# Performance work log

Hardware: AMD Instinct MI355X
Metric: run time of the kernel (lower is better)

## Reference

```python
import jax, jax.numpy as jnp
import numpy as np
from jax import lax

NEG = -1e9
B, H, C, TX, TY = 4, 256, 80, 256, 1024  # batch, hidden, mel bins, text len, mel len


def setup_inputs() -> dict:
    key = jax.random.key(0)
    k = jax.random.split(key, 6)
    en = jax.random.normal(k[0], (B, H, TX), jnp.float32)
    mu = jax.random.normal(k[1], (B, C, TX), jnp.float32)
    log_sigma = 0.1 * jax.random.normal(k[2], (B, C, TX), jnp.float32)
    y = jax.random.normal(k[3], (B, C, TY), jnp.float32)
    x_lengths = jax.random.randint(k[4], (B,), TX // 2, TX + 1, jnp.int32)
    y_lengths = jax.random.randint(k[5], (B,), TY // 2, TY + 1, jnp.int32)
    return {"en": en, "mu": mu, "log_sigma": log_sigma, "y": y,
            "x_lengths": x_lengths, "y_lengths": y_lengths}


def sequence_mask(lengths, max_len):
    return jnp.arange(max_len)[None, :] < lengths[:, None]


def compute_log_probs(mu, log_sigma, y):
    # y: [B,C,Ty] -> [B,1,Ty,C]; mu/log_sigma: [B,C,Tx] -> [B,Tx,1,C]
    yb = jnp.transpose(y, (0, 2, 1))[:, None]
    mub = jnp.transpose(mu, (0, 2, 1))[:, :, None]
    lsb = jnp.transpose(log_sigma, (0, 2, 1))[:, :, None]
    # mse / sigma^2 = (y-mu)^2 * exp(-2*log_sigma); mean over channel dim
    expo = -0.5 * jnp.mean((yb - mub) ** 2 * jnp.exp(-2.0 * lsb), axis=-1)  # [B,Tx,Ty]
    return expo - 0.5 * jnp.mean(lsb, axis=-1)  # broadcast [B,Tx,1] -> [B,Tx,Ty]


def maximum_path(logp, mask, x_lengths, y_lengths):
    """Monotonic alignment search (Glow-TTS Viterbi DP), vectorized over batch."""
    b, tx, ty = logp.shape
    lp = jnp.where(mask > 0, logp, NEG)
    cols = jnp.moveaxis(lp, 2, 0)  # [Ty, B, Tx]
    v0 = jnp.broadcast_to(jnp.where(jnp.arange(tx) == 0, 0.0, NEG), (b, tx)).astype(logp.dtype)

    def fwd(v, col):
        v_shift = jnp.concatenate([jnp.full((b, 1), NEG, v.dtype), v[:, :-1]], axis=1)
        diag = v_shift > v  # come from (x-1, y-1) rather than (x, y-1)
        return col + jnp.maximum(v, v_shift), diag

    _, diags = lax.scan(fwd, v0, cols)  # diags: [Ty, B, Tx] bool

    xs_idx = jnp.arange(tx)

    def bwd(idx, inp):
        yv, dcol = inp
        active = yv < y_lengths  # [B]
        row = (xs_idx[None, :] == idx[:, None]) & active[:, None]
        d = jnp.take_along_axis(dcol, idx[:, None], axis=1)[:, 0]
        idx = jnp.where(active & (idx > 0) & d, idx - 1, idx)
        return idx, row

    _, rows = lax.scan(bwd, x_lengths - 1, (jnp.arange(ty), diags), reverse=True)
    return lax.stop_gradient(jnp.moveaxis(rows, 0, 2).astype(logp.dtype))  # [B,Tx,Ty]


def generate_path(dr, mask):
    # dr: [B,Tx] durations; mask: [B,Tx,Ty]
    ty = mask.shape[-1]
    cum = jnp.cumsum(dr, axis=1)
    pm = (jnp.arange(ty)[None, None, :] < cum[:, :, None]).astype(dr.dtype)
    path = pm - jnp.pad(pm, ((0, 0), (1, 0), (0, 0)))[:, :-1]
    return path * mask


def reference(en, mu, log_sigma, y, x_lengths, y_lengths):
    tx, ty = mu.shape[-1], y.shape[-1]
    x_mask = sequence_mask(x_lengths, tx).astype(jnp.float32)  # [B,Tx]
    y_mask = sequence_mask(y_lengths, ty).astype(jnp.float32)  # [B,Ty]
    attn_mask = x_mask[:, :, None] * y_mask[:, None, :]        # [B,Tx,Ty]
    logp = compute_log_probs(mu, log_sigma, y)
    attn = maximum_path(logp, attn_mask, x_lengths, y_lengths)
    dr_mas = jnp.sum(attn, axis=-1)                            # durations [B,Tx]
    path = generate_path(dr_mas, attn_mask)                    # convert_dr_to_align
    # expand_encoder_outputs: attn^T @ en^T -> [B,H,Ty]
    o_en_ex = jnp.einsum('bxy,bhx->bhy', path, en)
    return o_en_ex, logp, attn, dr_mas
```

## Files before the change

### kernel.cpp

```cpp
#include <hip/hip_runtime.h>
#include <cstdint>
#include <cmath>

#define B_ 4
#define H_ 256
#define C_ 80
#define TX_ 256
#define TY_ 1024
#define NEGF (-1e9f)

#define OFF_LOGP (B_*H_*TY_)
#define OFF_ATTN (OFF_LOGP + B_*TX_*TY_)
#define OFF_DR   (OFF_ATTN + B_*TX_*TY_)

__device__ __forceinline__ float dpp_shr1_negfill_f32(float x) {
  union { float f; int i; } u, o, r;
  u.f = x; o.f = NEGF;
  r.i = __builtin_amdgcn_update_dpp(o.i, u.i, 0x138, 0xf, 0xf, false);
  return r.f;
}

__global__ __launch_bounds__(256) void k_logp(
    const float* __restrict__ mu, const float* __restrict__ ls,
    const float* __restrict__ y, const int* __restrict__ xlp,
    const int* __restrict__ ylp, float* __restrict__ logp_out,
    float* __restrict__ lpT)
{
  const int b  = blockIdx.y;
  const int x0 = blockIdx.x * 4;
  const int tid = threadIdx.x;
  __shared__ double s_w[4][C_];
  __shared__ double s_m1[4][C_];
  __shared__ double s_wm2[4][C_];
  __shared__ double s_lsv[4][C_];
  __shared__ double s_K[4];
  __shared__ double s_t0[4];
  __shared__ float tile[TY_][4];
  for (int i = tid; i < 4 * C_; i += 256) {
    int xi = i / C_, c = i - xi * C_;
    double m = (double)mu[(b * C_ + c) * TX_ + x0 + xi];
    double l = (double)ls[(b * C_ + c) * TX_ + x0 + xi];
    double w = exp(-2.0 * l);
    s_w[xi][c]   = w;
    s_m1[xi][c]  = -2.0 * w * m;
    s_wm2[xi][c] = w * m * m;
    s_lsv[xi][c] = l;
  }
  __syncthreads();
  {
    int xi = tid >> 6, cc = tid & 63;
    double kp = (cc < C_) ? s_wm2[xi][cc] : 0.0;
    double tp = (cc < C_) ? s_lsv[xi][cc] : 0.0;
    if (cc + 64 < C_) { kp += s_wm2[xi][cc + 64]; tp += s_lsv[xi][cc + 64]; }
#pragma unroll
    for (int off = 32; off; off >>= 1) {
      kp += __shfl_down(kp, off);
      tp += __shfl_down(tp, off);
    }
    if (cc == 0) { s_K[xi] = kp; s_t0[xi] = -0.5 * (tp * (1.0 / C_)); }
  }
  __syncthreads();

  const int t0 = tid * 4;
  double acc[4][4];
#pragma unroll
  for (int xi = 0; xi < 4; ++xi)
#pragma unroll
    for (int k = 0; k < 4; ++k) acc[xi][k] = 0.0;

  const float4* yp = (const float4*)(y + (size_t)b * C_ * TY_) + tid;
#pragma unroll 4
  for (int c = 0; c < C_; ++c) {
    float4 yv = yp[c * (TY_ / 4)];
    double y0 = yv.x, y1 = yv.y, y2 = yv.z, y3 = yv.w;
#pragma unroll
    for (int xi = 0; xi < 4; ++xi) {
      double w = s_w[xi][c], m1 = s_m1[xi][c];
      double u0 = fma(w, y0, m1), u1 = fma(w, y1, m1);
      double u2 = fma(w, y2, m1), u3 = fma(w, y3, m1);
      acc[xi][0] = fma(u0, y0, acc[xi][0]);
      acc[xi][1] = fma(u1, y1, acc[xi][1]);
      acc[xi][2] = fma(u2, y2, acc[xi][2]);
      acc[xi][3] = fma(u3, y3, acc[xi][3]);
    }
  }

  const int xlen = xlp[b], ylen = ylp[b];
#pragma unroll
  for (int xi = 0; xi < 4; ++xi) {
    int x = x0 + xi;
    double c0 = s_t0[xi], K = s_K[xi];
    float r[4];
#pragma unroll
    for (int k = 0; k < 4; ++k)
      r[k] = (float)((acc[xi][k] + K) * (-0.5 / C_) + c0);
    *(float4*)&logp_out[((size_t)(b * TX_ + x)) * TY_ + t0] =
        make_float4(r[0], r[1], r[2], r[3]);
    bool xm = x < xlen;
#pragma unroll
    for (int k = 0; k < 4; ++k)
      tile[t0 + k][xi] = (xm && (t0 + k) < ylen) ? r[k] : NEGF;
  }
  __syncthreads();

  float* dst = lpT + (size_t)b * TY_ * TX_ + x0;
  const float4* tp = (const float4*)tile;
#pragma unroll
  for (int k = 0; k < 4; ++k) {
    int t = tid + 256 * k;
    *(float4*)&dst[(size_t)t * TX_] = tp[t];
  }
}

__global__ __launch_bounds__(64, 1) void k_dp(
    const float* __restrict__ lpT, const int* __restrict__ xlp,
    const int* __restrict__ ylp, float* __restrict__ dr_out,
    int* __restrict__ cum_ws, int* __restrict__ xt_ws)
{
  const int b = blockIdx.x;
  const int tid = threadIdx.x;
  const int lane = tid;
  __shared__ __align__(16) uint32_t bits[8192];
  __shared__ __align__(16) uint32_t dur[TX_];

  const float4* gb4 = (const float4*)(lpT + (size_t)b * TY_ * TX_);

  float4 c[16];
#pragma unroll
  for (int i = 0; i < 16; ++i)
    c[i] = gb4[(size_t)i * (TX_ / 4) + lane];

  float v0 = (lane == 0) ? 0.0f : NEGF;
  float v1 = NEGF, v2 = NEGF, v3 = NEGF;
  uint32_t w0 = 0, w1 = 0, w2 = 0, w3 = 0;

  for (int g = 0; g < 32; ++g) {
#pragma unroll
    for (int u = 0; u < 32; ++u) {
      const int t = g * 32 + u;
      float4 col = c[u & 15];
      int tl = t + 16; tl = (tl > TY_ - 1) ? (TY_ - 1) : tl;
      c[u & 15] = gb4[(size_t)tl * (TX_ / 4) + lane];

      float sh = dpp_shr1_negfill_f32(v3);
      float m0 = fmaxf(v0, sh);
      float m1 = fmaxf(v1, v0);
      float m2 = fmaxf(v2, v1);
      float m3 = fmaxf(v3, v2);
      w0 |= (__float_as_uint(v0 - m0) >> 31) << u;
      w1 |= (__float_as_uint(v1 - m1) >> 31) << u;
      w2 |= (__float_as_uint(v2 - m2) >> 31) << u;
      w3 |= (__float_as_uint(v3 - m3) >> 31) << u;
      v0 = col.x + m0;
      v1 = col.y + m1;
      v2 = col.z + m2;
      v3 = col.w + m3;
    }
    *(uint4*)&bits[g * 256 + 4 * lane] = make_uint4(w0, w1, w2, w3);
    w0 = w1 = w2 = w3 = 0;
  }
  __syncthreads();

  *(uint4*)&dur[4 * tid] = make_uint4(0u, 0u, 0u, 0u);
  __syncthreads();

  const int xlen = xlp[b], ylen = ylp[b];
  if (tid == 0) {
    int idx = xlen - 1;
    int t = ylen - 1;
    while (t >= 0) {
      if (idx == 0) { dur[0] = (uint32_t)(t + 1); break; }
      int ww = t >> 5, rr = t & 31;
      uint32_t wd = bits[ww * 256 + idx];
      wd &= (rr == 31) ? 0xffffffffu : ((1u << (rr + 1)) - 1u);
      while (wd == 0 && ww > 0) { --ww; wd = bits[ww * 256 + idx]; }
      if (wd == 0) { dur[idx] = (uint32_t)(t + 1); break; }
      int bitpos = 31 - __builtin_clz(wd);
      int tp = (ww << 5) | bitpos;
      dur[idx] = (uint32_t)(t - tp + 1);
      --idx;
      t = tp - 1;
    }
  }
  __syncthreads();

  {
    uint32_t d0 = dur[4 * lane], d1 = dur[4 * lane + 1];
    uint32_t d2 = dur[4 * lane + 2], d3 = dur[4 * lane + 3];
    uint32_t own = d0 + d1 + d2 + d3;
    uint32_t s = own;
#pragma unroll
    for (int off = 1; off < 64; off <<= 1) {
      uint32_t n = __shfl_up(s, off);
      if (lane >= off) s += n;
    }
    uint32_t base = s - own;
    uint32_t c0 = base + d0, c1 = c0 + d1, c2 = c1 + d2, c3 = c2 + d3;
    int x = 4 * lane;
    cum_ws[b * TX_ + x]     = (int)c0;
    cum_ws[b * TX_ + x + 1] = (int)c1;
    cum_ws[b * TX_ + x + 2] = (int)c2;
    cum_ws[b * TX_ + x + 3] = (int)c3;
    dr_out[b * TX_ + x]     = (float)d0;
    dr_out[b * TX_ + x + 1] = (float)d1;
    dr_out[b * TX_ + x + 2] = (float)d2;
    dr_out[b * TX_ + x + 3] = (float)d3;
    int* xt = xt_ws + b * TY_;
    for (uint32_t t = c0 - d0; t < c0; ++t) xt[t] = x;
    for (uint32_t t = c1 - d1; t < c1; ++t) xt[t] = x + 1;
    for (uint32_t t = c2 - d2; t < c2; ++t) xt[t] = x + 2;
    for (uint32_t t = c3 - d3; t < c3; ++t) xt[t] = x + 3;
  }
}

__global__ __launch_bounds__(256) void k_epi(
    const int* __restrict__ cum_ws, const int* __restrict__ xt_ws,
    const float* __restrict__ en, const int* __restrict__ ylp,
    float* __restrict__ attn, float* __restrict__ oen)
{
  const int b = blockIdx.y, bx = blockIdx.x, tid = threadIdx.x;
  __shared__ float row[TX_];
  if (bx < TX_) {
    const int x = bx;
    int hi = cum_ws[b * TX_ + x];
    int lo = (x > 0) ? cum_ws[b * TX_ + x - 1] : 0;
    int t0 = tid * 4;
    float4 v;
    v.x = (t0     >= lo && t0     < hi) ? 1.f : 0.f;
    v.y = (t0 + 1 >= lo && t0 + 1 < hi) ? 1.f : 0.f;
    v.z = (t0 + 2 >= lo && t0 + 2 < hi) ? 1.f : 0.f;
    v.w = (t0 + 3 >= lo && t0 + 3 < hi) ? 1.f : 0.f;
    *(float4*)&attn[((size_t)(b * TX_ + x)) * TY_ + t0] = v;
  } else {
    const int h = bx - TX_;
    row[tid] = en[((size_t)(b * H_ + h)) * TX_ + tid];
    __syncthreads();
    const int ylen = ylp[b];
    int t0 = tid * 4;
    int4 xi = *(const int4*)&xt_ws[b * TY_ + t0];
    float4 v;
    v.x = (t0     < ylen) ? row[xi.x & (TX_ - 1)] : 0.f;
    v.y = (t0 + 1 < ylen) ? row[xi.y & (TX_ - 1)] : 0.f;
    v.z = (t0 + 2 < ylen) ? row[xi.z & (TX_ - 1)] : 0.f;
    v.w = (t0 + 3 < ylen) ? row[xi.w & (TX_ - 1)] : 0.f;
    *(float4*)&oen[((size_t)(b * H_ + h)) * TY_ + t0] = v;
  }
}

extern "C" void kernel_launch(void* const* d_in, const int* in_sizes, int n_in,
                              void* d_out, int out_size, void* d_ws, size_t ws_size,
                              hipStream_t stream)
{
  const float* en = (const float*)d_in[0];
  const float* mu = (const float*)d_in[1];
  const float* ls = (const float*)d_in[2];
  const float* y  = (const float*)d_in[3];
  const int*   xl = (const int*)d_in[4];
  const int*   yl = (const int*)d_in[5];

  float* out  = (float*)d_out;
  float* oen  = out;
  float* logp = out + OFF_LOGP;
  float* attn = out + OFF_ATTN;
  float* dr   = out + OFF_DR;

  int* cum = (int*)d_ws;
  int* xt  = cum + B_ * TX_;

  k_logp<<<dim3(TX_ / 4, B_),   256, 0, stream>>>(mu, ls, y, xl, yl, logp, attn);
  k_dp  <<<B_,                   64, 0, stream>>>(attn, xl, yl, dr, cum, xt);
  k_epi <<<dim3(TX_ + H_, B_),  256, 0, stream>>>(cum, xt, en, yl, attn, oen);
}
```

Before: 192.1 us.

## Warp-specialize DP kernel with producer warps staging columns into LDS ring

The Viterbi DP kernel grows from one wave to four. Three producer waves prefetch 32-column chunks of the transposed log-prob matrix from global memory into a triple-buffered shared-memory ring. The single consumer wave runs the serial recurrence and reads its columns from LDS, so it no longer waits on global loads. The cost is a block-wide barrier per 32-step chunk and about 96KB of extra shared memory.

Result: slower. 242.2 us (+26.1%).

```diff
diff --git a/kernel.cpp b/kernel.cpp
--- a/kernel.cpp
+++ b/kernel.cpp
@@ -112,56 +112,97 @@
   }
 }
 
-__global__ __launch_bounds__(64, 1) void k_dp(
+__global__ __launch_bounds__(256, 1) void k_dp(
     const float* __restrict__ lpT, const int* __restrict__ xlp,
     const int* __restrict__ ylp, float* __restrict__ dr_out,
     int* __restrict__ cum_ws, int* __restrict__ xt_ws)
 {
   const int b = blockIdx.x;
   const int tid = threadIdx.x;
-  const int lane = tid;
+  const int lane = tid & 63;
+  const int w = tid >> 6;
+  __shared__ __align__(16) float    ring[3 * 32 * 256];
   __shared__ __align__(16) uint32_t bits[8192];
   __shared__ __align__(16) uint32_t dur[TX_];
 
-  const float4* gb4 = (const float4*)(lpT + (size_t)b * TY_ * TX_);
-
-  float4 c[16];
-#pragma unroll
-  for (int i = 0; i < 16; ++i)
-    c[i] = gb4[(size_t)i * (TX_ / 4) + lane];
+  const float4* gb4   = (const float4*)(lpT + (size_t)b * TY_ * TX_);
+  const float4* ring4 = (const float4*)ring;
+
+  if (w != 0) {
+    const int p = w - 1;
+#pragma unroll
+    for (int c = 0; c < 2; ++c) {
+      float4 tmp[11];
+#pragma unroll
+      for (int i = 0; i < 11; ++i) {
+        int r = p + 3 * i;
+        if (r < 32) tmp[i] = gb4[(size_t)(c * 32 + r) * 64 + lane];
+      }
+      float4* dst = (float4*)&ring[c * 32 * 256];
+#pragma unroll
+      for (int i = 0; i < 11; ++i) {
+        int r = p + 3 * i;
+        if (r < 32) dst[r * 64 + lane] = tmp[i];
+      }
+    }
+  }
+  __syncthreads();
 
   float v0 = (lane == 0) ? 0.0f : NEGF;
   float v1 = NEGF, v2 = NEGF, v3 = NEGF;
   uint32_t w0 = 0, w1 = 0, w2 = 0, w3 = 0;
-
+  float4 rr[4];
+#pragma unroll
+  for (int i = 0; i < 4; ++i) rr[i] = ring4[i * 64 + lane];
+
+  int sA = 0, sB = 1;
   for (int g = 0; g < 32; ++g) {
-#pragma unroll
-    for (int u = 0; u < 32; ++u) {
-      const int t = g * 32 + u;
-      float4 col = c[u & 15];
-      int tl = t + 16; tl = (tl > TY_ - 1) ? (TY_ - 1) : tl;
-      c[u & 15] = gb4[(size_t)tl * (TX_ / 4) + lane];
-
-      float sh = dpp_shr1_negfill_f32(v3);
-      float m0 = fmaxf(v0, sh);
-      float m1 = fmaxf(v1, v0);
-      float m2 = fmaxf(v2, v1);
-      float m3 = fmaxf(v3, v2);
-      w0 |= (__float_as_uint(v0 - m0) >> 31) << u;
-      w1 |= (__float_as_uint(v1 - m1) >> 31) << u;
-      w2 |= (__float_as_uint(v2 - m2) >> 31) << u;
-      w3 |= (__float_as_uint(v3 - m3) >> 31) << u;
-      v0 = col.x + m0;
-      v1 = col.y + m1;
-      v2 = col.z + m2;
-      v3 = col.w + m3;
-    }
-    *(uint4*)&bits[g * 256 + 4 * lane] = make_uint4(w0, w1, w2, w3);
-    w0 = w1 = w2 = w3 = 0;
-  }
-  __syncthreads();
-
-  *(uint4*)&dur[4 * tid] = make_uint4(0u, 0u, 0u, 0u);
+    if (w == 0) {
+      const float4* bA = ring4 + sA * 2048;
+      const float4* bB = ring4 + sB * 2048;
+#pragma unroll
+      for (int u = 0; u < 32; ++u) {
+        float4 col = rr[u & 3];
+        if (u < 28) rr[u & 3] = bA[(u + 4) * 64 + lane];
+        else        rr[u & 3] = bB[(u - 28) * 64 + lane];
+
+        float sh = dpp_shr1_negfill_f32(v3);
+        float m0 = fmaxf(v0, sh);
+        float m1 = fmaxf(v1, v0);
+        float m2 = fmaxf(v2, v1);
+        float m3 = fmaxf(v3, v2);
+        w0 |= (__float_as_uint(v0 - m0) >> 31) << u;
+        w1 |= (__float_as_uint(v1 - m1) >> 31) << u;
+        w2 |= (__float_as_uint(v2 - m2) >> 31) << u;
+        w3 |= (__float_as_uint(v3 - m3) >> 31) << u;
+        v0 = col.x + m0;
+        v1 = col.y + m1;
+        v2 = col.z + m2;
+        v3 = col.w + m3;
+      }
+      *(uint4*)&bits[g * 256 + 4 * lane] = make_uint4(w0, w1, w2, w3);
+      w0 = w1 = w2 = w3 = 0;
+    } else if (g + 2 < 32) {
+      const int p = w - 1;
+      const int cbase = (g + 2) * 32;
+      float4* dst = (float4*)&ring[((g + 2) % 3) * 32 * 256];
+      float4 tmp[11];
+#pragma unroll
+      for (int i = 0; i < 11; ++i) {
+        int r = p + 3 * i;
+        if (r < 32) tmp[i] = gb4[(size_t)(cbase + r) * 64 + lane];
+      }
+#pragma unroll
+      for (int i = 0; i < 11; ++i) {
+        int r = p + 3 * i;
+        if (r < 32) dst[r * 64 + lane] = tmp[i];
+      }
+    }
+    __syncthreads();
+    sA = sB; sB = (sB == 2) ? 0 : sB + 1;
+  }
+
+  dur[tid] = 0;
   __syncthreads();
 
   const int xlen = xlp[b], ylen = ylp[b];
@@ -170,9 +211,9 @@
     int t = ylen - 1;
     while (t >= 0) {
       if (idx == 0) { dur[0] = (uint32_t)(t + 1); break; }
-      int ww = t >> 5, rr = t & 31;
+      int ww = t >> 5, rrm = t & 31;
       uint32_t wd = bits[ww * 256 + idx];
-      wd &= (rr == 31) ? 0xffffffffu : ((1u << (rr + 1)) - 1u);
+      wd &= (rrm == 31) ? 0xffffffffu : ((1u << (rrm + 1)) - 1u);
       while (wd == 0 && ww > 0) { --ww; wd = bits[ww * 256 + idx]; }
       if (wd == 0) { dur[idx] = (uint32_t)(t + 1); break; }
       int bitpos = 31 - __builtin_clz(wd);
@@ -184,7 +225,7 @@
   }
   __syncthreads();
 
-  {
+  if (w == 0) {
     uint32_t d0 = dur[4 * lane], d1 = dur[4 * lane + 1];
     uint32_t d2 = dur[4 * lane + 2], d3 = dur[4 * lane + 3];
     uint32_t own = d0 + d1 + d2 + d3;
@@ -268,6 +309,6 @@
   int* xt  = cum + B_ * TX_;
 
   k_logp<<<dim3(TX_ / 4, B_),   256, 0, stream>>>(mu, ls, y, xl, yl, logp, attn);
-  k_dp  <<<B_,                   64, 0, stream>>>(attn, xl, yl, dr, cum, xt);
+  k_dp  <<<B_,                  256, 0, stream>>>(attn, xl, yl, dr, cum, xt);
   k_epi <<<dim3(TX_ + H_, B_),  256, 0, stream>>>(cum, xt, en, yl, attn, oen);
 }
```

## Warp-specialize DP kernel with producer wavefronts staging columns into LDS ring

Applied to the files above, without the earlier changes.

The Viterbi DP kernel grows from one wavefront to four. Three producer wavefronts copy logp column chunks from global memory into a 6-slot LDS ring buffer and signal readiness through shared flags. The compute wavefront polls those flags and reads from LDS instead of issuing global loads on the serial critical path. The forward pass also stops at the chunk count set by ylen instead of always running 1024 steps. This aims to hide global memory latency in the sequential recurrence, at the cost of spin-wait synchronisation overhead and extra LDS use.

Measured after the change: 180.0 us. -6.3%, faster.

```diff
diff --git a/kernel.cpp b/kernel.cpp
--- a/kernel.cpp
+++ b/kernel.cpp
@@ -112,67 +112,121 @@
   }
 }
 
-__global__ __launch_bounds__(64, 1) void k_dp(
+#define POLL_FLAG(i)                                                     \
+  { while (vflag[i] == 0u) __builtin_amdgcn_s_sleep(1);                  \
+    asm volatile("" ::: "memory"); }
+
+#define DP_CHUNK(SHBASE)                                                 \
+  _Pragma("unroll")                                                      \
+  for (int u = 0; u < 16; ++u) {                                         \
+    float4 col = rr[u & 7];                                              \
+    rr[u & 7] = (u < 8) ? pA[(u + 8) * 64 + lane]                        \
+                        : pB[(u - 8) * 64 + lane];                       \
+    float sh = dpp_shr1_negfill_f32(v3);                                 \
+    float m0 = fmaxf(v0, sh);                                            \
+    float m1 = fmaxf(v1, v0);                                            \
+    float m2 = fmaxf(v2, v1);                                            \
+    float m3 = fmaxf(v3, v2);                                            \
+    w0 |= (__float_as_uint(v0 - m0) >> 31) << ((SHBASE) + u);            \
+    w1 |= (__float_as_uint(v1 - m1) >> 31) << ((SHBASE) + u);            \
+    w2 |= (__float_as_uint(v2 - m2) >> 31) << ((SHBASE) + u);            \
+    w3 |= (__float_as_uint(v3 - m3) >> 31) << ((SHBASE) + u);            \
+    v0 = col.x + m0;                                                     \
+    v1 = col.y + m1;                                                     \
+    v2 = col.z + m2;                                                     \
+    v3 = col.w + m3;                                                     \
+  }
+
+__global__ __launch_bounds__(256, 1) void k_dp(
     const float* __restrict__ lpT, const int* __restrict__ xlp,
     const int* __restrict__ ylp, float* __restrict__ dr_out,
     int* __restrict__ cum_ws, int* __restrict__ xt_ws)
 {
   const int b = blockIdx.x;
   const int tid = threadIdx.x;
-  const int lane = tid;
+  const int lane = tid & 63;
+  const int w = tid >> 6;
+  __shared__ __align__(16) float    ring[6 * 16 * 256];
   __shared__ __align__(16) uint32_t bits[8192];
   __shared__ __align__(16) uint32_t dur[TX_];
-
-  const float4* gb4 = (const float4*)(lpT + (size_t)b * TY_ * TX_);
-
-  float4 c[16];
-#pragma unroll
-  for (int i = 0; i < 16; ++i)
-    c[i] = gb4[(size_t)i * (TX_ / 4) + lane];
-
-  float v0 = (lane == 0) ? 0.0f : NEGF;
-  float v1 = NEGF, v2 = NEGF, v3 = NEGF;
-  uint32_t w0 = 0, w1 = 0, w2 = 0, w3 = 0;
-
-  for (int g = 0; g < 32; ++g) {
-#pragma unroll
-    for (int u = 0; u < 32; ++u) {
-      const int t = g * 32 + u;
-      float4 col = c[u & 15];
-      int tl = t + 16; tl = (tl > TY_ - 1) ? (TY_ - 1) : tl;
-      c[u & 15] = gb4[(size_t)tl * (TX_ / 4) + lane];
-
-      float sh = dpp_shr1_negfill_f32(v3);
-      float m0 = fmaxf(v0, sh);
-      float m1 = fmaxf(v1, v0);
-      float m2 = fmaxf(v2, v1);
-      float m3 = fmaxf(v3, v2);
-      w0 |= (__float_as_uint(v0 - m0) >> 31) << u;
-      w1 |= (__float_as_uint(v1 - m1) >> 31) << u;
-      w2 |= (__float_as_uint(v2 - m2) >> 31) << u;
-      w3 |= (__float_as_uint(v3 - m3) >> 31) << u;
-      v0 = col.x + m0;
-      v1 = col.y + m1;
-      v2 = col.z + m2;
-      v3 = col.w + m3;
-    }
-    *(uint4*)&bits[g * 256 + 4 * lane] = make_uint4(w0, w1, w2, w3);
-    w0 = w1 = w2 = w3 = 0;
-  }
-  __syncthreads();
-
-  *(uint4*)&dur[4 * tid] = make_uint4(0u, 0u, 0u, 0u);
-  __syncthreads();
-
-  const int xlen = xlp[b], ylen = ylp[b];
+  __shared__ uint32_t flags[64];
+  __shared__ int      prog;
+
+  const float4* gb4   = (const float4*)(lpT + (size_t)b * TY_ * TX_);
+  const float4* ring4 = (const float4*)ring;
+
+  const int ylen = ylp[b];
+  const int nch  = ((ylen + 31) >> 5) << 1;
+
+  if (tid < 64) flags[tid] = 0u;
+  if (tid == 0) prog = -1;
+  __syncthreads();
+
+  if (w == 0) {
+    volatile uint32_t* vflag = flags;
+    volatile int*      vprog = &prog;
+    POLL_FLAG(0);
+    float4 rr[8];
+#pragma unroll
+    for (int i = 0; i < 8; ++i) rr[i] = ring4[i * 64 + lane];
+
+    float v0 = (lane == 0) ? 0.0f : NEGF;
+    float v1 = NEGF, v2 = NEGF, v3 = NEGF;
+    uint32_t w0 = 0, w1 = 0, w2 = 0, w3 = 0;
+    int sA = 0, sB = 1;
+    const float4* pA;
+    const float4* pB;
+
+    for (int cp = 0; cp < nch; cp += 2) {
+      { int nf = (cp + 1 < nch) ? cp + 1 : nch - 1; POLL_FLAG(nf); }
+      pA = ring4 + sA * 1024; pB = ring4 + sB * 1024;
+      DP_CHUNK(0)
+      asm volatile("" ::: "memory");
+      *vprog = cp;
+      sA = sB; sB = (sB == 5) ? 0 : sB + 1;
+
+      { int nf = (cp + 2 < nch) ? cp + 2 : nch - 1; POLL_FLAG(nf); }
+      pA = ring4 + sA * 1024; pB = ring4 + sB * 1024;
+      DP_CHUNK(16)
+      *(uint4*)&bits[(cp >> 1) * 256 + 4 * lane] = make_uint4(w0, w1, w2, w3);
+      w0 = w1 = w2 = w3 = 0;
+      asm volatile("" ::: "memory");
+      *vprog = cp + 1;
+      sA = sB; sB = (sB == 5) ? 0 : sB + 1;
+    }
+  } else {
+    const int p = w - 1;
+    volatile int*      vprog = &prog;
+    volatile uint32_t* vflag = flags;
+    for (int c = p; c < nch; c += 3) {
+      const int need = c - 6;
+      while (*vprog < need) __builtin_amdgcn_s_sleep(8);
+      asm volatile("" ::: "memory");
+      const float4* src = gb4 + (size_t)(c * 16) * 64 + lane;
+      float4 tmp[16];
+#pragma unroll
+      for (int r = 0; r < 16; ++r) tmp[r] = src[r * 64];
+      float4* dst = (float4*)&ring[(c % 6) * 4096] + lane;
+#pragma unroll
+      for (int r = 0; r < 16; ++r) dst[r * 64] = tmp[r];
+      asm volatile("s_waitcnt lgkmcnt(0)" ::: "memory");
+      vflag[c] = 1u;
+    }
+  }
+
+  __syncthreads();
+  dur[tid] = 0;
+  __syncthreads();
+
+  const int xlen = xlp[b];
   if (tid == 0) {
     int idx = xlen - 1;
     int t = ylen - 1;
     while (t >= 0) {
       if (idx == 0) { dur[0] = (uint32_t)(t + 1); break; }
-      int ww = t >> 5, rr = t & 31;
+      int ww = t >> 5, rrm = t & 31;
       uint32_t wd = bits[ww * 256 + idx];
-      wd &= (rr == 31) ? 0xffffffffu : ((1u << (rr + 1)) - 1u);
+      wd &= (rrm == 31) ? 0xffffffffu : ((1u << (rrm + 1)) - 1u);
       while (wd == 0 && ww > 0) { --ww; wd = bits[ww * 256 + idx]; }
       if (wd == 0) { dur[idx] = (uint32_t)(t + 1); break; }
       int bitpos = 31 - __builtin_clz(wd);
@@ -184,7 +238,7 @@
   }
   __syncthreads();
 
-  {
+  if (w == 0) {
     uint32_t d0 = dur[4 * lane], d1 = dur[4 * lane + 1];
     uint32_t d2 = dur[4 * lane + 2], d3 = dur[4 * lane + 3];
     uint32_t own = d0 + d1 + d2 + d3;
@@ -268,6 +322,6 @@
   int* xt  = cum + B_ * TX_;
 
   k_logp<<<dim3(TX_ / 4, B_),   256, 0, stream>>>(mu, ls, y, xl, yl, logp, attn);
-  k_dp  <<<B_,                   64, 0, stream>>>(attn, xl, yl, dr, cum, xt);
+  k_dp  <<<B_,                  256, 0, stream>>>(attn, xl, yl, dr, cum, xt);
   k_epi <<<dim3(TX_ + H_, B_),  256, 0, stream>>>(cum, xt, en, yl, attn, oen);
 }
```
